# Kernel optimization log

Measured on AMD Instinct MI355X. Metric: run time of the kernel, lower is better.

## Reference

```python
import jax, jax.numpy as jnp
import numpy as np

V = 16384      # total nodes
G = 32         # nodes per graph (512 graphs)
D = 256        # node embedding dim == hidden_size
N = 8          # heads
H = 32         # head size
I = 1024       # intermediate size
LN_EPS = 1e-12


def _layer_norm(x, g, b):
    mu = jnp.mean(x, axis=-1, keepdims=True)
    var = jnp.mean(jnp.square(x - mu), axis=-1, keepdims=True)
    return (x - mu) * jax.lax.rsqrt(var + LN_EPS) * g + b


def setup_inputs() -> dict:
    key = jax.random.key(0)
    ks = jax.random.split(key, 5)
    node_embeddings = jax.random.normal(ks[0], (V, D), jnp.float32)
    # fully-connected pairs within each graph of size G (sorted by source node)
    idx = np.arange(V, dtype=np.int32).reshape(-1, G)          # [num_graphs, G]
    src = np.repeat(idx, G, axis=1).reshape(-1)                # [P]
    dst = np.tile(idx, (1, G)).reshape(-1)                     # [P]
    in_graph_node_pairs = jnp.asarray(np.stack([src, dst], axis=-1))  # [P, 2]
    s = 0.02
    return {
        "node_embeddings": node_embeddings,
        "in_graph_node_pairs": in_graph_node_pairs,
        "W_qkv": jax.random.normal(ks[1], (D, 3 * N * H), jnp.float32) * s,
        "W_o": jax.random.normal(ks[2], (N * H, D), jnp.float32) * s,
        "ln1_g": jnp.ones((D,), jnp.float32),
        "ln1_b": jnp.zeros((D,), jnp.float32),
        "W_i": jax.random.normal(ks[3], (D, I), jnp.float32) * s,
        "W_out2": jax.random.normal(ks[4], (I, D), jnp.float32) * s,
        "ln2_g": jnp.ones((D,), jnp.float32),
        "ln2_b": jnp.zeros((D,), jnp.float32),
    }


def reference(node_embeddings, in_graph_node_pairs, W_qkv, W_o, ln1_g, ln1_b,
              W_i, W_out2, ln2_g, ln2_b):
    nV = node_embeddings.shape[0]
    src = in_graph_node_pairs[:, 0]
    dst = in_graph_node_pairs[:, 1]
    # QKV projection -> [V, N, 3H] -> split
    qkv = (node_embeddings @ W_qkv).reshape(nV, N, 3 * H)
    q, k, v = jnp.split(qkv, 3, axis=-1)                       # each [V, N, H]
    # per-pair scores [P, N]
    scores = jnp.einsum('phi,phi->ph', q[src], k[dst]) / jnp.sqrt(jnp.float32(H))
    # segment softmax over source node, all heads at once
    m = jax.ops.segment_max(scores, src, num_segments=nV)       # [V, N]
    e = jnp.exp(scores - m[src])
    denom = jax.ops.segment_sum(e, src, num_segments=nV)        # [V, N]
    w = e / denom[src]                                          # [P, N]
    # weighted value scatter-sum -> [V, N, H]
    wv = w[:, :, None] * v[dst]
    att = jax.ops.segment_sum(wv, src, num_segments=nV).reshape(nV, N * H)
    # output projection + residual + LN
    pre = _layer_norm(att @ W_o + node_embeddings, ln1_g, ln1_b)
    inter = jax.nn.gelu(pre @ W_i, approximate=False)
    out = _layer_norm(inter @ W_out2 + pre, ln2_g, ln2_b)
    return out
```

## Files before the change

### kernel.cpp

```cpp
#include <hip/hip_runtime.h>
#include <math.h>

#define V 16384
#define D 256
#define NH 256
#define THREE_NH 768
#define IDIM 1024
#define LN_EPS 1e-12f
#define SCL 0.17677669529663687f

typedef short s16x8 __attribute__((ext_vector_type(8)));
typedef float f32x4 __attribute__((ext_vector_type(4)));

__device__ inline unsigned short f2bf(float f) {
    unsigned u = __float_as_uint(f);
    u += 0x7fffu + ((u >> 16) & 1u);
    return (unsigned short)(u >> 16);
}
__device__ inline float bf2f(unsigned short s) {
    return __uint_as_float(((unsigned)s) << 16);
}

__device__ inline float fast_erf(float x) {
    float ax = fabsf(x);
    float t  = 1.f / fmaf(0.3275911f, ax, 1.f);
    float p  = fmaf(fmaf(fmaf(fmaf(1.061405429f, t, -1.453152027f), t,
                              1.421413741f), t, -0.284496736f), t, 0.254829592f);
    float e  = 1.f - p * t * __expf(-ax * ax);
    return copysignf(e, x);
}

__device__ inline void gl2lds16(const unsigned short* g, unsigned short* l) {
    __builtin_amdgcn_global_load_lds(
        (__attribute__((address_space(1))) void*)(g),
        (__attribute__((address_space(3))) void*)(l), 16, 0, 0);
}

template <int ROWS_T>
__device__ inline void stage(const unsigned short* __restrict__ src, size_t row0,
                             int ldk, int k0, unsigned short* lds, int wv, int lane) {
    constexpr int PER_WAVE = ROWS_T / 32;
    #pragma unroll
    for (int i = 0; i < PER_WAVE; ++i) {
        const int seg = wv * PER_WAVE + i;
        const int r = seg * 8 + (lane >> 3);
        const int c = (lane & 7) ^ (r & 7);
        gl2lds16(src + (row0 + (size_t)r) * ldk + k0 + c * 8, lds + seg * 512);
    }
}

__device__ inline void stage_wp(const unsigned short* __restrict__ src, size_t row0,
                                int ldk, int k0, unsigned short* seg, int lane) {
    #pragma unroll
    for (int i = 0; i < 8; ++i) {
        const int r = i * 8 + (lane >> 3);
        const int c = (lane & 7) ^ (r & 7);
        gl2lds16(src + (row0 + (size_t)r) * ldk + k0 + c * 8, seg + i * 512);
    }
}

__device__ inline s16x8 fragld(const unsigned short* lds, int row, int chunk) {
    return *(const s16x8*)&lds[row * 64 + ((chunk ^ (row & 7)) << 3)];
}

#define WAVE_LGKM0() do { asm volatile("s_waitcnt lgkmcnt(0)" ::: "memory"); \
                          __builtin_amdgcn_sched_barrier(0); } while (0)
#define WAVE_VM0()   do { asm volatile("s_waitcnt vmcnt(0)" ::: "memory");   \
                          __builtin_amdgcn_sched_barrier(0); } while (0)

__global__ __launch_bounds__(256) void prep(const float* __restrict__ X,
                                            unsigned short* __restrict__ Xb,
                                            const float* __restrict__ Wqkv,
                                            const float* __restrict__ Wo,
                                            const float* __restrict__ Wi,
                                            const float* __restrict__ Wo2,
                                            unsigned short* __restrict__ WqkvT,
                                            unsigned short* __restrict__ WoT,
                                            unsigned short* __restrict__ WiT,
                                            unsigned short* __restrict__ Wo2T) {
    const int b = blockIdx.x, t = threadIdx.x;
    if (b >= 768) {
        int i = (b - 768) * 256 + t;
        float4 v = ((const float4*)X)[i];
        ushort4 o;
        o.x = f2bf(v.x); o.y = f2bf(v.y); o.z = f2bf(v.z); o.w = f2bf(v.w);
        ((ushort4*)Xb)[i] = o;
        return;
    }
    __shared__ float tile[32][33];
    const float* W; unsigned short* Wt; int K, N, bx, by;
    if (b < 192)      { W = Wqkv; Wt = WqkvT; K = 256;  N = 768;  bx = b & 7;          by = b >> 3; }
    else if (b < 256) { W = Wo;   Wt = WoT;   K = 256;  N = 256;  bx = (b - 192) & 7;  by = (b - 192) >> 3; }
    else if (b < 512) { W = Wi;   Wt = WiT;   K = 256;  N = 1024; bx = (b - 256) & 7;  by = (b - 256) >> 3; }
    else              { W = Wo2;  Wt = Wo2T;  K = 1024; N = 256;  bx = (b - 512) & 31; by = (b - 512) >> 5; }
    const int k0 = bx * 32, n0 = by * 32;
    #pragma unroll
    for (int p = 0; p < 4; ++p) {
        int idx = t + p * 256, r = idx >> 5, c = idx & 31;
        tile[r][c] = W[(size_t)(k0 + r) * N + n0 + c];
    }
    __syncthreads();
    #pragma unroll
    for (int p = 0; p < 4; ++p) {
        int idx = t + p * 256, r = idx >> 5, c = idx & 31;
        Wt[(size_t)(n0 + r) * K + k0 + c] = f2bf(tile[c][r]);
    }
}

template <int K, int N, int EPI>
__global__ __launch_bounds__(256) void gemm128(const unsigned short* __restrict__ A,
                                               const unsigned short* __restrict__ Bt,
                                               unsigned short* __restrict__ C) {
    __shared__ unsigned short As[128 * 64];
    __shared__ unsigned short Bs[128 * 64];
    constexpr int NCOL = N / 128;
    const int b = blockIdx.x;
    const int idx = b >> 3;
    const int r0 = ((b & 7) * 16 + idx / NCOL) * 128;
    const int c0 = (idx % NCOL) * 128;
    const int t = threadIdx.x;
    const int wv = t >> 6, lane = t & 63, q = lane >> 4, l16 = lane & 15;
    const int wr = (wv >> 1) * 64, wc = (wv & 1) * 64;
    f32x4 acc[4][4] = {};

    for (int k0 = 0; k0 < K; k0 += 64) {
        __syncthreads();
        stage<128>(A,  (size_t)r0, K, k0, As, wv, lane);
        stage<128>(Bt, (size_t)c0, K, k0, Bs, wv, lane);
        __builtin_amdgcn_s_waitcnt(0);
        __syncthreads();
        #pragma unroll
        for (int kk2 = 0; kk2 < 2; ++kk2) {
            s16x8 af[4], bfr[4];
            #pragma unroll
            for (int mf = 0; mf < 4; ++mf)
                af[mf] = fragld(As, wr + mf * 16 + l16, kk2 * 4 + q);
            #pragma unroll
            for (int nf = 0; nf < 4; ++nf)
                bfr[nf] = fragld(Bs, wc + nf * 16 + l16, kk2 * 4 + q);
            #pragma unroll
            for (int mf = 0; mf < 4; ++mf)
                #pragma unroll
                for (int nf = 0; nf < 4; ++nf)
                    acc[mf][nf] = __builtin_amdgcn_mfma_f32_16x16x32_bf16(af[mf], bfr[nf], acc[mf][nf], 0, 0, 0);
        }
    }

    #pragma unroll
    for (int mf = 0; mf < 4; ++mf)
        #pragma unroll
        for (int nf = 0; nf < 4; ++nf) {
            const int cg = c0 + wc + nf * 16 + l16;
            #pragma unroll
            for (int r = 0; r < 4; ++r) {
                const int rg = r0 + wr + mf * 16 + q * 4 + r;
                float v = acc[mf][nf][r];
                if (EPI == 1) v = 0.5f * v * (1.f + fast_erf(v * 0.70710678118654752f));
                C[(size_t)rg * N + cg] = f2bf(v);
            }
        }
}

__device__ inline void ffn_mfma8(const unsigned short* At, const unsigned short* Bb,
                                 int l16, int q, f32x4 (&acc)[2][4]) {
    #pragma unroll
    for (int kk2 = 0; kk2 < 2; ++kk2) {
        s16x8 af[2], bv[4];
        #pragma unroll
        for (int mf = 0; mf < 2; ++mf)
            af[mf] = fragld(At, mf * 16 + l16, kk2 * 4 + q);
        #pragma unroll
        for (int nf = 0; nf < 4; ++nf)
            bv[nf] = fragld(Bb, nf * 16 + l16, kk2 * 4 + q);
        #pragma unroll
        for (int mf = 0; mf < 2; ++mf)
            #pragma unroll
            for (int nf = 0; nf < 4; ++nf)
                acc[mf][nf] = __builtin_amdgcn_mfma_f32_16x16x32_bf16(af[mf], bv[nf], acc[mf][nf], 0, 0, 0);
    }
}

__global__ __launch_bounds__(256) void ffn_ln(const unsigned short* __restrict__ preb,
                                              const unsigned short* __restrict__ WiT,
                                              const unsigned short* __restrict__ Wo2T,
                                              const float* __restrict__ gamma,
                                              const float* __restrict__ beta,
                                              float* __restrict__ out) {
    __shared__ unsigned short Apre[8192];
    __shared__ unsigned short Bs[16384];
    __shared__ unsigned short Pbuf[8192];
    __shared__ float2 partial[4][32];
    __shared__ float2 stats[32];
    const int t = threadIdx.x, r0 = blockIdx.x * 32;
    const int wv = t >> 6, lane = t & 63, q = lane >> 4, l16 = lane & 15;
    const int wc = wv * 64;
    unsigned short* Bseg = Bs + wv * 4096;
    f32x4 acc2[2][4] = {};

    #pragma unroll
    for (int kc = 0; kc < 4; ++kc)
        stage<32>(preb, (size_t)r0, 256, kc * 64, Apre + kc * 2048, wv, lane);
    stage_wp(WiT, (size_t)wc, 256, 0, Bseg, lane);
    __builtin_amdgcn_s_waitcnt(0);
    __syncthreads();

    for (int nc = 0; nc < 4; ++nc) {
        const int ncn = (nc + 1) & 3;
        f32x4 acc1[2][4] = {};

        #pragma unroll
        for (int k0 = 0; k0 < 256; k0 += 64) {
            WAVE_VM0();
            ffn_mfma8(Apre + (k0 >> 6) * 2048, Bseg, l16, q, acc1);
            WAVE_LGKM0();
            if (k0 < 192)
                stage_wp(WiT, (size_t)(nc * 256 + wc), 256, k0 + 64, Bseg, lane);
            else
                stage_wp(Wo2T, (size_t)wc, IDIM, nc * 256, Bseg, lane);
        }

        #pragma unroll
        for (int mf = 0; mf < 2; ++mf)
            #pragma unroll
            for (int nf = 0; nf < 4; ++nf)
                #pragma unroll
                for (int r = 0; r < 4; ++r) {
                    float v = acc1[mf][nf][r];
                    v = 0.5f * v * (1.f + fast_erf(v * 0.70710678118654752f));
                    const int i = mf * 16 + q * 4 + r;
                    const int colc = wc + nf * 16 + l16;
                    const int c8 = (colc >> 3) & 7;
                    Pbuf[wv * 2048 + i * 64 + ((c8 ^ (i & 7)) << 3) + (colc & 7)] = f2bf(v);
                }
        __syncthreads();

        #pragma unroll
        for (int ks = 0; ks < 256; ks += 64) {
            WAVE_VM0();
            ffn_mfma8(Pbuf + (ks >> 6) * 2048, Bseg, l16, q, acc2);
            WAVE_LGKM0();
            if (ks < 192)
                stage_wp(Wo2T, (size_t)wc, IDIM, nc * 256 + ks + 64, Bseg, lane);
            else
                stage_wp(WiT, (size_t)(ncn * 256 + wc), 256, 0, Bseg, lane);
        }
        __syncthreads();
    }

    #pragma unroll
    for (int mf = 0; mf < 2; ++mf)
        #pragma unroll
        for (int nf = 0; nf < 4; ++nf) {
            const int cg = wc + nf * 16 + l16;
            const int kb = cg >> 6, c8 = (cg >> 3) & 7, e = cg & 7;
            #pragma unroll
            for (int r = 0; r < 4; ++r) {
                const int i = mf * 16 + q * 4 + r;
                acc2[mf][nf][r] += bf2f(Apre[kb * 2048 + i * 64 + ((c8 ^ (i & 7)) << 3) + e]);
            }
        }

    #pragma unroll
    for (int mf = 0; mf < 2; ++mf) {
        float s[4] = {0.f, 0.f, 0.f, 0.f}, ss[4] = {0.f, 0.f, 0.f, 0.f};
        #pragma unroll
        for (int nf = 0; nf < 4; ++nf)
            #pragma unroll
            for (int r = 0; r < 4; ++r) {
                float v = acc2[mf][nf][r];
                s[r] += v; ss[r] += v * v;
            }
        #pragma unroll
        for (int off = 1; off < 16; off <<= 1)
            #pragma unroll
            for (int r = 0; r < 4; ++r) {
                s[r]  += __shfl_xor(s[r],  off);
                ss[r] += __shfl_xor(ss[r], off);
            }
        if (l16 == 0)
            #pragma unroll
            for (int r = 0; r < 4; ++r)
                partial[wv][mf * 16 + q * 4 + r] = make_float2(s[r], ss[r]);
    }
    __syncthreads();
    if (t < 32) {
        float s = 0.f, ss = 0.f;
        #pragma unroll
        for (int w = 0; w < 4; ++w) { s += partial[w][t].x; ss += partial[w][t].y; }
        float mu  = s * (1.f / 256.f);
        float var = ss * (1.f / 256.f) - mu * mu;
        stats[t] = make_float2(mu, rsqrtf(var + LN_EPS));
    }
    __syncthreads();

    #pragma unroll
    for (int mf = 0; mf < 2; ++mf)
        #pragma unroll
        for (int nf = 0; nf < 4; ++nf) {
            const int cg = wc + nf * 16 + l16;
            const float g = gamma[cg], b = beta[cg];
            #pragma unroll
            for (int r = 0; r < 4; ++r) {
                const int rl = mf * 16 + q * 4 + r;
                const float2 st = stats[rl];
                out[(size_t)(r0 + rl) * NH + cg] = (acc2[mf][nf][r] - st.x) * st.y * g + b;
            }
        }
}

__global__ __launch_bounds__(256) void attln(const unsigned short* __restrict__ qkv,
                                             const unsigned short* __restrict__ WoT,
                                             const float* __restrict__ X,
                                             const float* __restrict__ gamma,
                                             const float* __restrict__ beta,
                                             unsigned short* __restrict__ preb) {
    __shared__ unsigned short smem[25216];
    unsigned short* Ks = smem;
    unsigned short* Vt = smem + 8192;
    unsigned short* Ps = smem + 16384;
    unsigned short* at = smem;
    unsigned short* Bs = smem + 8192;
    float2* partial = (float2*)(smem + 24576);
    float2* stats   = (float2*)(smem + 24576 + 512);

    const int g = blockIdx.x, t = threadIdx.x;
    const int wv = t >> 6, lane = t & 63, q = lane >> 4, l16 = lane & 15;
    const unsigned short* src = qkv + (size_t)g * 32 * THREE_NH;

    s16x8 qf[2][2];
    #pragma unroll
    for (int hh = 0; hh < 2; ++hh)
        #pragma unroll
        for (int mf = 0; mf < 2; ++mf)
            qf[hh][mf] = *(const s16x8*)&src[(size_t)(mf * 16 + l16) * THREE_NH +
                                             (wv * 2 + hh) * 96 + q * 8];

    s16x8 vld[4];
    int vh[4], vj[4], vdc[4];
    #pragma unroll
    for (int i = 0; i < 4; ++i) {
        int cid = i * 256 + t;
        vh[i] = cid >> 7; int rem = cid & 127; vj[i] = rem >> 2; vdc[i] = rem & 3;
        vld[i] = *(const s16x8*)&src[(size_t)vj[i] * THREE_NH + vh[i] * 96 + 64 + vdc[i] * 8];
    }

    #pragma unroll
    for (int i = 0; i < 4; ++i) {
        int ck = (wv * 4 + i) * 64 + lane;
        int h = ck >> 7, j = (ck >> 2) & 31, c = ck & 3;
        gl2lds16(src + (size_t)j * THREE_NH + h * 96 + 32 + c * 8, Ks + (wv * 4 + i) * 512);
    }

    #pragma unroll
    for (int i = 0; i < 4; ++i)
        #pragma unroll
        for (int e = 0; e < 8; ++e) {
            int d = vdc[i] * 8 + e;
            Vt[vh[i] * 1024 + d * 32 + ((((vj[i] >> 3) ^ ((d >> 2) & 3))) << 3) + (vj[i] & 7)] =
                (unsigned short)vld[i][e];
        }

    __builtin_amdgcn_s_waitcnt(0);
    __syncthreads();

    f32x4 sacc[2][2][2] = {};
    #pragma unroll
    for (int hh = 0; hh < 2; ++hh) {
        const int h = wv * 2 + hh;
        #pragma unroll
        for (int nf = 0; nf < 2; ++nf) {
            s16x8 kf = *(const s16x8*)&Ks[h * 1024 + (nf * 16 + l16) * 32 + q * 8];
            #pragma unroll
            for (int mf = 0; mf < 2; ++mf)
                sacc[hh][mf][nf] = __builtin_amdgcn_mfma_f32_16x16x32_bf16(
                    qf[hh][mf], kf, sacc[hh][mf][nf], 0, 0, 0);
        }
    }

    float inv[2][2][4];
    #pragma unroll
    for (int hh = 0; hh < 2; ++hh) {
        const int h = wv * 2 + hh;
        #pragma unroll
        for (int mf = 0; mf < 2; ++mf)
            #pragma unroll
            for (int r = 0; r < 4; ++r) {
                float a0 = sacc[hh][mf][0][r], a1 = sacc[hh][mf][1][r];
                float m = fmaxf(a0, a1);
                m = fmaxf(m, __shfl_xor(m, 1));
                m = fmaxf(m, __shfl_xor(m, 2));
                m = fmaxf(m, __shfl_xor(m, 4));
                m = fmaxf(m, __shfl_xor(m, 8));
                float e0 = __expf((a0 - m) * SCL);
                float e1 = __expf((a1 - m) * SCL);
                float sm = e0 + e1;
                sm += __shfl_xor(sm, 1);
                sm += __shfl_xor(sm, 2);
                sm += __shfl_xor(sm, 4);
                sm += __shfl_xor(sm, 8);
                inv[hh][mf][r] = 1.f / sm;
                const int row = mf * 16 + q * 4 + r;
                const int base = h * 1024 + row * 32 + (l16 & 7);
                Ps[base + ((((l16 >> 3) ^ q)) << 3)]       = f2bf(e0);
                Ps[base + ((((2 + (l16 >> 3)) ^ q)) << 3)] = f2bf(e1);
            }
    }

    f32x4 oacc[2][2][2] = {};
    #pragma unroll
    for (int hh = 0; hh < 2; ++hh) {
        const int h = wv * 2 + hh;
        const int sw = (l16 >> 2) & 3;
        s16x8 pa[2], vb[2];
        #pragma unroll
        for (int mf = 0; mf < 2; ++mf)
            pa[mf] = *(const s16x8*)&Ps[h * 1024 + (mf * 16 + l16) * 32 + ((q ^ sw) << 3)];
        #pragma unroll
        for (int nf = 0; nf < 2; ++nf)
            vb[nf] = *(const s16x8*)&Vt[h * 1024 + (nf * 16 + l16) * 32 + ((q ^ sw) << 3)];
        #pragma unroll
        for (int mf = 0; mf < 2; ++mf)
            #pragma unroll
            for (int nf = 0; nf < 2; ++nf)
                oacc[hh][mf][nf] = __builtin_amdgcn_mfma_f32_16x16x32_bf16(
                    pa[mf], vb[nf], oacc[hh][mf][nf], 0, 0, 0);
    }
    __syncthreads();

    const int wc = wv * 64;
    unsigned short* Bseg = Bs + wv * 4096;
    stage_wp(WoT, (size_t)wc, 256, 0, Bseg, lane);

    #pragma unroll
    for (int hh = 0; hh < 2; ++hh)
        #pragma unroll
        for (int mf = 0; mf < 2; ++mf)
            #pragma unroll
            for (int nf = 0; nf < 2; ++nf)
                #pragma unroll
                for (int r = 0; r < 4; ++r) {
                    float val = oacc[hh][mf][nf][r] * inv[hh][mf][r];
                    const int i = mf * 16 + q * 4 + r;
                    const int col = (wv * 2 + hh) * 32 + nf * 16 + l16;
                    const int kb = col >> 6, c = (col >> 3) & 7;
                    at[kb * 2048 + i * 64 + ((c ^ (i & 7)) << 3) + (col & 7)] = f2bf(val);
                }
    __syncthreads();

    const int r0 = g * 32;
    f32x4 acc[2][4] = {};

    #pragma unroll
    for (int kc = 0; kc < 4; ++kc) {
        WAVE_VM0();
        const unsigned short* atk = at + kc * 2048;
        #pragma unroll
        for (int kk2 = 0; kk2 < 2; ++kk2) {
            s16x8 af[2], bv[4];
            #pragma unroll
            for (int mf = 0; mf < 2; ++mf)
                af[mf] = fragld(atk, mf * 16 + l16, kk2 * 4 + q);
            #pragma unroll
            for (int nf = 0; nf < 4; ++nf)
                bv[nf] = fragld(Bseg, nf * 16 + l16, kk2 * 4 + q);
            #pragma unroll
            for (int mf = 0; mf < 2; ++mf)
                #pragma unroll
                for (int nf = 0; nf < 4; ++nf)
                    acc[mf][nf] = __builtin_amdgcn_mfma_f32_16x16x32_bf16(af[mf], bv[nf], acc[mf][nf], 0, 0, 0);
        }
        if (kc < 3) {
            WAVE_LGKM0();
            stage_wp(WoT, (size_t)wc, 256, (kc + 1) * 64, Bseg, lane);
        }
    }

    #pragma unroll
    for (int mf = 0; mf < 2; ++mf)
        #pragma unroll
        for (int nf = 0; nf < 4; ++nf) {
            const int cg = wc + nf * 16 + l16;
            #pragma unroll
            for (int r = 0; r < 4; ++r)
                acc[mf][nf][r] += X[(size_t)(r0 + mf * 16 + q * 4 + r) * NH + cg];
        }

    #pragma unroll
    for (int mf = 0; mf < 2; ++mf) {
        float sp[4] = {0.f, 0.f, 0.f, 0.f}, ssp[4] = {0.f, 0.f, 0.f, 0.f};
        #pragma unroll
        for (int nf = 0; nf < 4; ++nf)
            #pragma unroll
            for (int r = 0; r < 4; ++r) {
                float v = acc[mf][nf][r];
                sp[r] += v; ssp[r] += v * v;
            }
        #pragma unroll
        for (int off = 1; off < 16; off <<= 1)
            #pragma unroll
            for (int r = 0; r < 4; ++r) {
                sp[r]  += __shfl_xor(sp[r],  off);
                ssp[r] += __shfl_xor(ssp[r], off);
            }
        if (l16 == 0)
            #pragma unroll
            for (int r = 0; r < 4; ++r)
                partial[wv * 32 + mf * 16 + q * 4 + r] = make_float2(sp[r], ssp[r]);
    }
    __syncthreads();
    if (t < 32) {
        float sv = 0.f, ssv = 0.f;
        #pragma unroll
        for (int w = 0; w < 4; ++w) { sv += partial[w * 32 + t].x; ssv += partial[w * 32 + t].y; }
        float mu  = sv * (1.f / 256.f);
        float var = ssv * (1.f / 256.f) - mu * mu;
        stats[t] = make_float2(mu, rsqrtf(var + LN_EPS));
    }
    __syncthreads();

    #pragma unroll
    for (int mf = 0; mf < 2; ++mf)
        #pragma unroll
        for (int nf = 0; nf < 4; ++nf) {
            const int cg = wc + nf * 16 + l16;
            const float gm = gamma[cg], bt = beta[cg];
            #pragma unroll
            for (int r = 0; r < 4; ++r) {
                const int rl = mf * 16 + q * 4 + r;
                const float2 st = stats[rl];
                float v = (acc[mf][nf][r] - st.x) * st.y * gm + bt;
                preb[(size_t)(r0 + rl) * NH + cg] = f2bf(v);
            }
        }
}

extern "C" void kernel_launch(void* const* d_in, const int* in_sizes, int n_in,
                              void* d_out, int out_size, void* d_ws, size_t ws_size,
                              hipStream_t stream) {
    const float* X      = (const float*)d_in[0];
    const float* W_qkv  = (const float*)d_in[2];
    const float* W_o    = (const float*)d_in[3];
    const float* ln1_g  = (const float*)d_in[4];
    const float* ln1_b  = (const float*)d_in[5];
    const float* W_i    = (const float*)d_in[6];
    const float* W_out2 = (const float*)d_in[7];
    const float* ln2_g  = (const float*)d_in[8];
    const float* ln2_b  = (const float*)d_in[9];
    float* out = (float*)d_out;

    char* ws = (char*)d_ws;
    unsigned short* Xbf   = (unsigned short*)(ws);
    unsigned short* qkvb  = (unsigned short*)(ws + 8388608);
    unsigned short* preb  = (unsigned short*)(ws + 58720256);
    unsigned short* WqkvT = (unsigned short*)(ws + 67108864);
    unsigned short* WoT   = (unsigned short*)(ws + 67502080);
    unsigned short* WiT   = (unsigned short*)(ws + 67633152);
    unsigned short* Wo2T  = (unsigned short*)(ws + 68157440);

    dim3 blk(256);
    hipLaunchKernelGGL(prep, dim3(768 + V * D / 4 / 256), blk, 0, stream,
                       X, Xbf, W_qkv, W_o, W_i, W_out2, WqkvT, WoT, WiT, Wo2T);

    hipLaunchKernelGGL((gemm128<D, THREE_NH, 0>), dim3(V / 128 * (THREE_NH / 128)), blk, 0, stream,
                       Xbf, WqkvT, qkvb);
    hipLaunchKernelGGL(attln, dim3(V / 32), blk, 0, stream,
                       qkvb, WoT, X, ln1_g, ln1_b, preb);
    hipLaunchKernelGGL(ffn_ln, dim3(V / 32), blk, 0, stream,
                       preb, WiT, Wo2T, ln2_g, ln2_b, out);
}
```

Before: 153.7 us.

## Split fused FFN+LN kernel across eight waves with 32-column slices

The fused FFN/LayerNorm kernel now launches 512 threads per block instead of 256, so each of eight waves owns a 32-column slice instead of a 64-column slice. Per-wave weight staging, MFMA tiles, the GELU buffer indexing and the LN partial reduction are all adjusted to match. The goal is more waves in flight to hide global-to-LDS latency and raise MFMA utilisation. In exchange each wave reuses its A fragments across fewer columns, and per-block LDS use stays the same while the thread count doubles.

```diff
diff --git a/kernel.cpp b/kernel.cpp
--- a/kernel.cpp
+++ b/kernel.cpp
@@ -53,6 +53,16 @@
                                 int ldk, int k0, unsigned short* seg, int lane) {
     #pragma unroll
     for (int i = 0; i < 8; ++i) {
+        const int r = i * 8 + (lane >> 3);
+        const int c = (lane & 7) ^ (r & 7);
+        gl2lds16(src + (row0 + (size_t)r) * ldk + k0 + c * 8, seg + i * 512);
+    }
+}
+
+__device__ inline void stage_wp32(const unsigned short* __restrict__ src, size_t row0,
+                                  int ldk, int k0, unsigned short* seg, int lane) {
+    #pragma unroll
+    for (int i = 0; i < 4; ++i) {
         const int r = i * 8 + (lane >> 3);
         const int c = (lane & 7) ^ (r & 7);
         gl2lds16(src + (row0 + (size_t)r) * ldk + k0 + c * 8, seg + i * 512);
@@ -161,26 +171,26 @@
         }
 }
 
-__device__ inline void ffn_mfma8(const unsigned short* At, const unsigned short* Bb,
-                                 int l16, int q, f32x4 (&acc)[2][4]) {
+__device__ inline void ffn_mfma4(const unsigned short* At, const unsigned short* Bb,
+                                 int l16, int q, f32x4 (&acc)[2][2]) {
     #pragma unroll
     for (int kk2 = 0; kk2 < 2; ++kk2) {
-        s16x8 af[2], bv[4];
+        s16x8 af[2], bv[2];
         #pragma unroll
         for (int mf = 0; mf < 2; ++mf)
             af[mf] = fragld(At, mf * 16 + l16, kk2 * 4 + q);
         #pragma unroll
-        for (int nf = 0; nf < 4; ++nf)
+        for (int nf = 0; nf < 2; ++nf)
             bv[nf] = fragld(Bb, nf * 16 + l16, kk2 * 4 + q);
         #pragma unroll
         for (int mf = 0; mf < 2; ++mf)
             #pragma unroll
-            for (int nf = 0; nf < 4; ++nf)
+            for (int nf = 0; nf < 2; ++nf)
                 acc[mf][nf] = __builtin_amdgcn_mfma_f32_16x16x32_bf16(af[mf], bv[nf], acc[mf][nf], 0, 0, 0);
     }
 }
 
-__global__ __launch_bounds__(256) void ffn_ln(const unsigned short* __restrict__ preb,
+__global__ __launch_bounds__(512) void ffn_ln(const unsigned short* __restrict__ preb,
                                               const unsigned short* __restrict__ WiT,
                                               const unsigned short* __restrict__ Wo2T,
                                               const float* __restrict__ gamma,
@@ -189,60 +199,65 @@
     __shared__ unsigned short Apre[8192];
     __shared__ unsigned short Bs[16384];
     __shared__ unsigned short Pbuf[8192];
-    __shared__ float2 partial[4][32];
+    __shared__ float2 partial[8][32];
     __shared__ float2 stats[32];
     const int t = threadIdx.x, r0 = blockIdx.x * 32;
     const int wv = t >> 6, lane = t & 63, q = lane >> 4, l16 = lane & 15;
-    const int wc = wv * 64;
-    unsigned short* Bseg = Bs + wv * 4096;
-    f32x4 acc2[2][4] = {};
-
-    #pragma unroll
-    for (int kc = 0; kc < 4; ++kc)
-        stage<32>(preb, (size_t)r0, 256, kc * 64, Apre + kc * 2048, wv, lane);
-    stage_wp(WiT, (size_t)wc, 256, 0, Bseg, lane);
+    const int wc = wv * 32;
+    unsigned short* Bseg = Bs + wv * 2048;
+    f32x4 acc2[2][2] = {};
+
+    #pragma unroll
+    for (int i = 0; i < 2; ++i) {
+        const int seg = wv * 2 + i;
+        const int kb = seg >> 2, sub = seg & 3;
+        const int r = sub * 8 + (lane >> 3);
+        const int c = (lane & 7) ^ (r & 7);
+        gl2lds16(preb + (size_t)(r0 + r) * 256 + kb * 64 + c * 8, Apre + seg * 512);
+    }
+    stage_wp32(WiT, (size_t)wc, 256, 0, Bseg, lane);
     __builtin_amdgcn_s_waitcnt(0);
     __syncthreads();
 
     for (int nc = 0; nc < 4; ++nc) {
         const int ncn = (nc + 1) & 3;
-        f32x4 acc1[2][4] = {};
+        f32x4 acc1[2][2] = {};
 
         #pragma unroll
         for (int k0 = 0; k0 < 256; k0 += 64) {
             WAVE_VM0();
-            ffn_mfma8(Apre + (k0 >> 6) * 2048, Bseg, l16, q, acc1);
+            ffn_mfma4(Apre + (k0 >> 6) * 2048, Bseg, l16, q, acc1);
             WAVE_LGKM0();
             if (k0 < 192)
-                stage_wp(WiT, (size_t)(nc * 256 + wc), 256, k0 + 64, Bseg, lane);
+                stage_wp32(WiT, (size_t)(nc * 256 + wc), 256, k0 + 64, Bseg, lane);
             else
-                stage_wp(Wo2T, (size_t)wc, IDIM, nc * 256, Bseg, lane);
-        }
-
-        #pragma unroll
-        for (int mf = 0; mf < 2; ++mf)
-            #pragma unroll
-            for (int nf = 0; nf < 4; ++nf)
+                stage_wp32(Wo2T, (size_t)wc, IDIM, nc * 256, Bseg, lane);
+        }
+
+        #pragma unroll
+        for (int mf = 0; mf < 2; ++mf)
+            #pragma unroll
+            for (int nf = 0; nf < 2; ++nf)
                 #pragma unroll
                 for (int r = 0; r < 4; ++r) {
                     float v = acc1[mf][nf][r];
                     v = 0.5f * v * (1.f + fast_erf(v * 0.70710678118654752f));
                     const int i = mf * 16 + q * 4 + r;
                     const int colc = wc + nf * 16 + l16;
-                    const int c8 = (colc >> 3) & 7;
-                    Pbuf[wv * 2048 + i * 64 + ((c8 ^ (i & 7)) << 3) + (colc & 7)] = f2bf(v);
+                    Pbuf[(colc >> 6) * 2048 + i * 64 +
+                         ((((colc >> 3) & 7) ^ (i & 7)) << 3) + (colc & 7)] = f2bf(v);
                 }
         __syncthreads();
 
         #pragma unroll
         for (int ks = 0; ks < 256; ks += 64) {
             WAVE_VM0();
-            ffn_mfma8(Pbuf + (ks >> 6) * 2048, Bseg, l16, q, acc2);
+            ffn_mfma4(Pbuf + (ks >> 6) * 2048, Bseg, l16, q, acc2);
             WAVE_LGKM0();
             if (ks < 192)
-                stage_wp(Wo2T, (size_t)wc, IDIM, nc * 256 + ks + 64, Bseg, lane);
+                stage_wp32(Wo2T, (size_t)wc, IDIM, nc * 256 + ks + 64, Bseg, lane);
             else
-                stage_wp(WiT, (size_t)(ncn * 256 + wc), 256, 0, Bseg, lane);
+                stage_wp32(WiT, (size_t)(ncn * 256 + wc), 256, 0, Bseg, lane);
         }
         __syncthreads();
     }
@@ -250,7 +265,7 @@
     #pragma unroll
     for (int mf = 0; mf < 2; ++mf)
         #pragma unroll
-        for (int nf = 0; nf < 4; ++nf) {
+        for (int nf = 0; nf < 2; ++nf) {
             const int cg = wc + nf * 16 + l16;
             const int kb = cg >> 6, c8 = (cg >> 3) & 7, e = cg & 7;
             #pragma unroll
@@ -264,7 +279,7 @@
     for (int mf = 0; mf < 2; ++mf) {
         float s[4] = {0.f, 0.f, 0.f, 0.f}, ss[4] = {0.f, 0.f, 0.f, 0.f};
         #pragma unroll
-        for (int nf = 0; nf < 4; ++nf)
+        for (int nf = 0; nf < 2; ++nf)
             #pragma unroll
             for (int r = 0; r < 4; ++r) {
                 float v = acc2[mf][nf][r];
@@ -286,7 +301,7 @@
     if (t < 32) {
         float s = 0.f, ss = 0.f;
         #pragma unroll
-        for (int w = 0; w < 4; ++w) { s += partial[w][t].x; ss += partial[w][t].y; }
+        for (int w = 0; w < 8; ++w) { s += partial[w][t].x; ss += partial[w][t].y; }
         float mu  = s * (1.f / 256.f);
         float var = ss * (1.f / 256.f) - mu * mu;
         stats[t] = make_float2(mu, rsqrtf(var + LN_EPS));
@@ -296,7 +311,7 @@
     #pragma unroll
     for (int mf = 0; mf < 2; ++mf)
         #pragma unroll
-        for (int nf = 0; nf < 4; ++nf) {
+        for (int nf = 0; nf < 2; ++nf) {
             const int cg = wc + nf * 16 + l16;
             const float g = gamma[cg], b = beta[cg];
             #pragma unroll
@@ -565,6 +580,6 @@
                        Xbf, WqkvT, qkvb);
     hipLaunchKernelGGL(attln, dim3(V / 32), blk, 0, stream,
                        qkvb, WoT, X, ln1_g, ln1_b, preb);
-    hipLaunchKernelGGL(ffn_ln, dim3(V / 32), blk, 0, stream,
+    hipLaunchKernelGGL(ffn_ln, dim3(V / 32), dim3(512), 0, stream,
                        preb, WiT, Wo2T, ln2_g, ln2_b, out);
 }
```

Measured after the change: 167.2 us. +8.8%, slower.

## Fuse attention+LN1 kernel with FFN+LN2 kernel into one per-graph kernel

Applied to the files above, without the earlier changes.

Merges the attention/output-projection/LN1 kernel and the FFN/LN2 kernel into a single kernel. The normalized pre-FFN activation stays in shared memory as bf16 instead of being written to and reread from global memory, and one launch is removed. Shared memory per block grows from about 50KB to about 67KB, which may lower occupancy, and the fused kernel may use more registers.

```diff
diff --git a/kernel.cpp b/kernel.cpp
--- a/kernel.cpp
+++ b/kernel.cpp
@@ -180,152 +180,35 @@
     }
 }
 
-__global__ __launch_bounds__(256) void ffn_ln(const unsigned short* __restrict__ preb,
+__global__ __launch_bounds__(256) void attffn(const unsigned short* __restrict__ qkv,
+                                              const unsigned short* __restrict__ WoT,
+                                              const float* __restrict__ X,
+                                              const float* __restrict__ ln1g,
+                                              const float* __restrict__ ln1b,
                                               const unsigned short* __restrict__ WiT,
                                               const unsigned short* __restrict__ Wo2T,
-                                              const float* __restrict__ gamma,
-                                              const float* __restrict__ beta,
+                                              const float* __restrict__ ln2g,
+                                              const float* __restrict__ ln2b,
                                               float* __restrict__ out) {
-    __shared__ unsigned short Apre[8192];
-    __shared__ unsigned short Bs[16384];
-    __shared__ unsigned short Pbuf[8192];
-    __shared__ float2 partial[4][32];
-    __shared__ float2 stats[32];
-    const int t = threadIdx.x, r0 = blockIdx.x * 32;
-    const int wv = t >> 6, lane = t & 63, q = lane >> 4, l16 = lane & 15;
-    const int wc = wv * 64;
-    unsigned short* Bseg = Bs + wv * 4096;
-    f32x4 acc2[2][4] = {};
-
-    #pragma unroll
-    for (int kc = 0; kc < 4; ++kc)
-        stage<32>(preb, (size_t)r0, 256, kc * 64, Apre + kc * 2048, wv, lane);
-    stage_wp(WiT, (size_t)wc, 256, 0, Bseg, lane);
-    __builtin_amdgcn_s_waitcnt(0);
-    __syncthreads();
-
-    for (int nc = 0; nc < 4; ++nc) {
-        const int ncn = (nc + 1) & 3;
-        f32x4 acc1[2][4] = {};
-
-        #pragma unroll
-        for (int k0 = 0; k0 < 256; k0 += 64) {
-            WAVE_VM0();
-            ffn_mfma8(Apre + (k0 >> 6) * 2048, Bseg, l16, q, acc1);
-            WAVE_LGKM0();
-            if (k0 < 192)
-                stage_wp(WiT, (size_t)(nc * 256 + wc), 256, k0 + 64, Bseg, lane);
-            else
-                stage_wp(Wo2T, (size_t)wc, IDIM, nc * 256, Bseg, lane);
-        }
-
-        #pragma unroll
-        for (int mf = 0; mf < 2; ++mf)
-            #pragma unroll
-            for (int nf = 0; nf < 4; ++nf)
-                #pragma unroll
-                for (int r = 0; r < 4; ++r) {
-                    float v = acc1[mf][nf][r];
-                    v = 0.5f * v * (1.f + fast_erf(v * 0.70710678118654752f));
-                    const int i = mf * 16 + q * 4 + r;
-                    const int colc = wc + nf * 16 + l16;
-                    const int c8 = (colc >> 3) & 7;
-                    Pbuf[wv * 2048 + i * 64 + ((c8 ^ (i & 7)) << 3) + (colc & 7)] = f2bf(v);
-                }
-        __syncthreads();
-
-        #pragma unroll
-        for (int ks = 0; ks < 256; ks += 64) {
-            WAVE_VM0();
-            ffn_mfma8(Pbuf + (ks >> 6) * 2048, Bseg, l16, q, acc2);
-            WAVE_LGKM0();
-            if (ks < 192)
-                stage_wp(Wo2T, (size_t)wc, IDIM, nc * 256 + ks + 64, Bseg, lane);
-            else
-                stage_wp(WiT, (size_t)(ncn * 256 + wc), 256, 0, Bseg, lane);
-        }
-        __syncthreads();
-    }
-
-    #pragma unroll
-    for (int mf = 0; mf < 2; ++mf)
-        #pragma unroll
-        for (int nf = 0; nf < 4; ++nf) {
-            const int cg = wc + nf * 16 + l16;
-            const int kb = cg >> 6, c8 = (cg >> 3) & 7, e = cg & 7;
-            #pragma unroll
-            for (int r = 0; r < 4; ++r) {
-                const int i = mf * 16 + q * 4 + r;
-                acc2[mf][nf][r] += bf2f(Apre[kb * 2048 + i * 64 + ((c8 ^ (i & 7)) << 3) + e]);
-            }
-        }
-
-    #pragma unroll
-    for (int mf = 0; mf < 2; ++mf) {
-        float s[4] = {0.f, 0.f, 0.f, 0.f}, ss[4] = {0.f, 0.f, 0.f, 0.f};
-        #pragma unroll
-        for (int nf = 0; nf < 4; ++nf)
-            #pragma unroll
-            for (int r = 0; r < 4; ++r) {
-                float v = acc2[mf][nf][r];
-                s[r] += v; ss[r] += v * v;
-            }
-        #pragma unroll
-        for (int off = 1; off < 16; off <<= 1)
-            #pragma unroll
-            for (int r = 0; r < 4; ++r) {
-                s[r]  += __shfl_xor(s[r],  off);
-                ss[r] += __shfl_xor(ss[r], off);
-            }
-        if (l16 == 0)
-            #pragma unroll
-            for (int r = 0; r < 4; ++r)
-                partial[wv][mf * 16 + q * 4 + r] = make_float2(s[r], ss[r]);
-    }
-    __syncthreads();
-    if (t < 32) {
-        float s = 0.f, ss = 0.f;
-        #pragma unroll
-        for (int w = 0; w < 4; ++w) { s += partial[w][t].x; ss += partial[w][t].y; }
-        float mu  = s * (1.f / 256.f);
-        float var = ss * (1.f / 256.f) - mu * mu;
-        stats[t] = make_float2(mu, rsqrtf(var + LN_EPS));
-    }
-    __syncthreads();
-
-    #pragma unroll
-    for (int mf = 0; mf < 2; ++mf)
-        #pragma unroll
-        for (int nf = 0; nf < 4; ++nf) {
-            const int cg = wc + nf * 16 + l16;
-            const float g = gamma[cg], b = beta[cg];
-            #pragma unroll
-            for (int r = 0; r < 4; ++r) {
-                const int rl = mf * 16 + q * 4 + r;
-                const float2 st = stats[rl];
-                out[(size_t)(r0 + rl) * NH + cg] = (acc2[mf][nf][r] - st.x) * st.y * g + b;
-            }
-        }
-}
-
-__global__ __launch_bounds__(256) void attln(const unsigned short* __restrict__ qkv,
-                                             const unsigned short* __restrict__ WoT,
-                                             const float* __restrict__ X,
-                                             const float* __restrict__ gamma,
-                                             const float* __restrict__ beta,
-                                             unsigned short* __restrict__ preb) {
-    __shared__ unsigned short smem[25216];
+    __shared__ unsigned short smem[33408];
     unsigned short* Ks = smem;
     unsigned short* Vt = smem + 8192;
     unsigned short* Ps = smem + 16384;
     unsigned short* at = smem;
-    unsigned short* Bs = smem + 8192;
-    float2* partial = (float2*)(smem + 24576);
-    float2* stats   = (float2*)(smem + 24576 + 512);
+    unsigned short* Bsp = smem + 8192;
+    unsigned short* Apre = smem;
+    unsigned short* Pbuf = smem + 24576;
+    float2* partial1 = (float2*)(smem + 24576);
+    float2* stats1   = (float2*)(smem + 24576 + 512);
+    float2* partial2 = (float2*)(smem + 32768);
+    float2* stats2   = (float2*)(smem + 32768 + 512);
 
     const int g = blockIdx.x, t = threadIdx.x;
     const int wv = t >> 6, lane = t & 63, q = lane >> 4, l16 = lane & 15;
     const unsigned short* src = qkv + (size_t)g * 32 * THREE_NH;
+    const int wc = wv * 64;
+    const int r0 = g * 32;
+    unsigned short* Bseg = Bsp + wv * 4096;
 
     s16x8 qf[2][2];
     #pragma unroll
@@ -427,8 +310,6 @@
     }
     __syncthreads();
 
-    const int wc = wv * 64;
-    unsigned short* Bseg = Bs + wv * 4096;
     stage_wp(WoT, (size_t)wc, 256, 0, Bseg, lane);
 
     #pragma unroll
@@ -447,32 +328,139 @@
                 }
     __syncthreads();
 
-    const int r0 = g * 32;
-    f32x4 acc[2][4] = {};
-
-    #pragma unroll
-    for (int kc = 0; kc < 4; ++kc) {
-        WAVE_VM0();
-        const unsigned short* atk = at + kc * 2048;
-        #pragma unroll
-        for (int kk2 = 0; kk2 < 2; ++kk2) {
-            s16x8 af[2], bv[4];
-            #pragma unroll
-            for (int mf = 0; mf < 2; ++mf)
-                af[mf] = fragld(atk, mf * 16 + l16, kk2 * 4 + q);
+    {
+        f32x4 acc[2][4] = {};
+        #pragma unroll
+        for (int kc = 0; kc < 4; ++kc) {
+            WAVE_VM0();
+            const unsigned short* atk = at + kc * 2048;
+            #pragma unroll
+            for (int kk2 = 0; kk2 < 2; ++kk2) {
+                s16x8 af[2], bv[4];
+                #pragma unroll
+                for (int mf = 0; mf < 2; ++mf)
+                    af[mf] = fragld(atk, mf * 16 + l16, kk2 * 4 + q);
+                #pragma unroll
+                for (int nf = 0; nf < 4; ++nf)
+                    bv[nf] = fragld(Bseg, nf * 16 + l16, kk2 * 4 + q);
+                #pragma unroll
+                for (int mf = 0; mf < 2; ++mf)
+                    #pragma unroll
+                    for (int nf = 0; nf < 4; ++nf)
+                        acc[mf][nf] = __builtin_amdgcn_mfma_f32_16x16x32_bf16(af[mf], bv[nf], acc[mf][nf], 0, 0, 0);
+            }
+            if (kc < 3) {
+                WAVE_LGKM0();
+                stage_wp(WoT, (size_t)wc, 256, (kc + 1) * 64, Bseg, lane);
+            }
+        }
+
+        #pragma unroll
+        for (int mf = 0; mf < 2; ++mf)
+            #pragma unroll
+            for (int nf = 0; nf < 4; ++nf) {
+                const int cg = wc + nf * 16 + l16;
+                #pragma unroll
+                for (int r = 0; r < 4; ++r)
+                    acc[mf][nf][r] += X[(size_t)(r0 + mf * 16 + q * 4 + r) * NH + cg];
+            }
+
+        #pragma unroll
+        for (int mf = 0; mf < 2; ++mf) {
+            float sp[4] = {0.f, 0.f, 0.f, 0.f}, ssp[4] = {0.f, 0.f, 0.f, 0.f};
             #pragma unroll
             for (int nf = 0; nf < 4; ++nf)
-                bv[nf] = fragld(Bseg, nf * 16 + l16, kk2 * 4 + q);
-            #pragma unroll
-            for (int mf = 0; mf < 2; ++mf)
-                #pragma unroll
-                for (int nf = 0; nf < 4; ++nf)
-                    acc[mf][nf] = __builtin_amdgcn_mfma_f32_16x16x32_bf16(af[mf], bv[nf], acc[mf][nf], 0, 0, 0);
-        }
-        if (kc < 3) {
+                #pragma unroll
+                for (int r = 0; r < 4; ++r) {
+                    float v = acc[mf][nf][r];
+                    sp[r] += v; ssp[r] += v * v;
+                }
+            #pragma unroll
+            for (int off = 1; off < 16; off <<= 1)
+                #pragma unroll
+                for (int r = 0; r < 4; ++r) {
+                    sp[r]  += __shfl_xor(sp[r],  off);
+                    ssp[r] += __shfl_xor(ssp[r], off);
+                }
+            if (l16 == 0)
+                #pragma unroll
+                for (int r = 0; r < 4; ++r)
+                    partial1[wv * 32 + mf * 16 + q * 4 + r] = make_float2(sp[r], ssp[r]);
+        }
+        __syncthreads();
+        if (t < 32) {
+            float sv = 0.f, ssv = 0.f;
+            #pragma unroll
+            for (int w = 0; w < 4; ++w) { sv += partial1[w * 32 + t].x; ssv += partial1[w * 32 + t].y; }
+            float mu  = sv * (1.f / 256.f);
+            float var = ssv * (1.f / 256.f) - mu * mu;
+            stats1[t] = make_float2(mu, rsqrtf(var + LN_EPS));
+        }
+        __syncthreads();
+
+        #pragma unroll
+        for (int mf = 0; mf < 2; ++mf)
+            #pragma unroll
+            for (int nf = 0; nf < 4; ++nf) {
+                const int cg = wc + nf * 16 + l16;
+                const float gm = ln1g[cg], bt = ln1b[cg];
+                const int kb = cg >> 6, c8 = (cg >> 3) & 7, e = cg & 7;
+                #pragma unroll
+                for (int r = 0; r < 4; ++r) {
+                    const int i = mf * 16 + q * 4 + r;
+                    const float2 st = stats1[i];
+                    float v = (acc[mf][nf][r] - st.x) * st.y * gm + bt;
+                    Apre[kb * 2048 + i * 64 + ((c8 ^ (i & 7)) << 3) + e] = f2bf(v);
+                }
+            }
+    }
+    stage_wp(WiT, (size_t)wc, 256, 0, Bseg, lane);
+    WAVE_LGKM0();
+    __builtin_amdgcn_s_barrier();
+    __builtin_amdgcn_sched_barrier(0);
+
+    f32x4 acc2[2][4] = {};
+    for (int nc = 0; nc < 4; ++nc) {
+        const int ncn = (nc + 1) & 3;
+        f32x4 acc1[2][4] = {};
+
+        #pragma unroll
+        for (int k0 = 0; k0 < 256; k0 += 64) {
+            WAVE_VM0();
+            ffn_mfma8(Apre + (k0 >> 6) * 2048, Bseg, l16, q, acc1);
             WAVE_LGKM0();
-            stage_wp(WoT, (size_t)wc, 256, (kc + 1) * 64, Bseg, lane);
-        }
+            if (k0 < 192)
+                stage_wp(WiT, (size_t)(nc * 256 + wc), 256, k0 + 64, Bseg, lane);
+            else
+                stage_wp(Wo2T, (size_t)wc, IDIM, nc * 256, Bseg, lane);
+        }
+
+        #pragma unroll
+        for (int mf = 0; mf < 2; ++mf)
+            #pragma unroll
+            for (int nf = 0; nf < 4; ++nf)
+                #pragma unroll
+                for (int r = 0; r < 4; ++r) {
+                    float v = acc1[mf][nf][r];
+                    v = 0.5f * v * (1.f + fast_erf(v * 0.70710678118654752f));
+                    const int i = mf * 16 + q * 4 + r;
+                    const int colc = wc + nf * 16 + l16;
+                    const int c8 = (colc >> 3) & 7;
+                    Pbuf[wv * 2048 + i * 64 + ((c8 ^ (i & 7)) << 3) + (colc & 7)] = f2bf(v);
+                }
+        __syncthreads();
+
+        #pragma unroll
+        for (int ks = 0; ks < 256; ks += 64) {
+            WAVE_VM0();
+            ffn_mfma8(Pbuf + (ks >> 6) * 2048, Bseg, l16, q, acc2);
+            WAVE_LGKM0();
+            if (ks < 192)
+                stage_wp(Wo2T, (size_t)wc, IDIM, nc * 256 + ks + 64, Bseg, lane);
+            else
+                stage_wp(WiT, (size_t)(ncn * 256 + wc), 256, 0, Bseg, lane);
+        }
+        __syncthreads();
     }
 
     #pragma unroll
@@ -480,41 +468,44 @@
         #pragma unroll
         for (int nf = 0; nf < 4; ++nf) {
             const int cg = wc + nf * 16 + l16;
+            const int kb = cg >> 6, c8 = (cg >> 3) & 7, e = cg & 7;
+            #pragma unroll
+            for (int r = 0; r < 4; ++r) {
+                const int i = mf * 16 + q * 4 + r;
+                acc2[mf][nf][r] += bf2f(Apre[kb * 2048 + i * 64 + ((c8 ^ (i & 7)) << 3) + e]);
+            }
+        }
+
+    #pragma unroll
+    for (int mf = 0; mf < 2; ++mf) {
+        float s[4] = {0.f, 0.f, 0.f, 0.f}, ss[4] = {0.f, 0.f, 0.f, 0.f};
+        #pragma unroll
+        for (int nf = 0; nf < 4; ++nf)
+            #pragma unroll
+            for (int r = 0; r < 4; ++r) {
+                float v = acc2[mf][nf][r];
+                s[r] += v; ss[r] += v * v;
+            }
+        #pragma unroll
+        for (int off = 1; off < 16; off <<= 1)
+            #pragma unroll
+            for (int r = 0; r < 4; ++r) {
+                s[r]  += __shfl_xor(s[r],  off);
+                ss[r] += __shfl_xor(ss[r], off);
+            }
+        if (l16 == 0)
             #pragma unroll
             for (int r = 0; r < 4; ++r)
-                acc[mf][nf][r] += X[(size_t)(r0 + mf * 16 + q * 4 + r) * NH + cg];
-        }
-
-    #pragma unroll
-    for (int mf = 0; mf < 2; ++mf) {
-        float sp[4] = {0.f, 0.f, 0.f, 0.f}, ssp[4] = {0.f, 0.f, 0.f, 0.f};
-        #pragma unroll
-        for (int nf = 0; nf < 4; ++nf)
-            #pragma unroll
-            for (int r = 0; r < 4; ++r) {
-                float v = acc[mf][nf][r];
-                sp[r] += v; ssp[r] += v * v;
-            }
-        #pragma unroll
-        for (int off = 1; off < 16; off <<= 1)
-            #pragma unroll
-            for (int r = 0; r < 4; ++r) {
-                sp[r]  += __shfl_xor(sp[r],  off);
-                ssp[r] += __shfl_xor(ssp[r], off);
-            }
-        if (l16 == 0)
-            #pragma unroll
-            for (int r = 0; r < 4; ++r)
-                partial[wv * 32 + mf * 16 + q * 4 + r] = make_float2(sp[r], ssp[r]);
+                partial2[wv * 32 + mf * 16 + q * 4 + r] = make_float2(s[r], ss[r]);
     }
     __syncthreads();
     if (t < 32) {
-        float sv = 0.f, ssv = 0.f;
-        #pragma unroll
-        for (int w = 0; w < 4; ++w) { sv += partial[w * 32 + t].x; ssv += partial[w * 32 + t].y; }
-        float mu  = sv * (1.f / 256.f);
-        float var = ssv * (1.f / 256.f) - mu * mu;
-        stats[t] = make_float2(mu, rsqrtf(var + LN_EPS));
+        float s = 0.f, ss = 0.f;
+        #pragma unroll
+        for (int w = 0; w < 4; ++w) { s += partial2[w * 32 + t].x; ss += partial2[w * 32 + t].y; }
+        float mu  = s * (1.f / 256.f);
+        float var = ss * (1.f / 256.f) - mu * mu;
+        stats2[t] = make_float2(mu, rsqrtf(var + LN_EPS));
     }
     __syncthreads();
 
@@ -523,13 +514,12 @@
         #pragma unroll
         for (int nf = 0; nf < 4; ++nf) {
             const int cg = wc + nf * 16 + l16;
-            const float gm = gamma[cg], bt = beta[cg];
+            const float gm = ln2g[cg], bt = ln2b[cg];
             #pragma unroll
             for (int r = 0; r < 4; ++r) {
                 const int rl = mf * 16 + q * 4 + r;
-                const float2 st = stats[rl];
-                float v = (acc[mf][nf][r] - st.x) * st.y * gm + bt;
-                preb[(size_t)(r0 + rl) * NH + cg] = f2bf(v);
+                const float2 st = stats2[rl];
+                out[(size_t)(r0 + rl) * NH + cg] = (acc2[mf][nf][r] - st.x) * st.y * gm + bt;
             }
         }
 }
@@ -551,7 +541,6 @@
     char* ws = (char*)d_ws;
     unsigned short* Xbf   = (unsigned short*)(ws);
     unsigned short* qkvb  = (unsigned short*)(ws + 8388608);
-    unsigned short* preb  = (unsigned short*)(ws + 58720256);
     unsigned short* WqkvT = (unsigned short*)(ws + 67108864);
     unsigned short* WoT   = (unsigned short*)(ws + 67502080);
     unsigned short* WiT   = (unsigned short*)(ws + 67633152);
@@ -563,8 +552,6 @@
 
     hipLaunchKernelGGL((gemm128<D, THREE_NH, 0>), dim3(V / 128 * (THREE_NH / 128)), blk, 0, stream,
                        Xbf, WqkvT, qkvb);
-    hipLaunchKernelGGL(attln, dim3(V / 32), blk, 0, stream,
-                       qkvb, WoT, X, ln1_g, ln1_b, preb);
-    hipLaunchKernelGGL(ffn_ln, dim3(V / 32), blk, 0, stream,
-                       preb, WiT, Wo2T, ln2_g, ln2_b, out);
-}
+    hipLaunchKernelGGL(attffn, dim3(V / 32), blk, 0, stream,
+                       qkvb, WoT, X, ln1_g, ln1_b, WiT, Wo2T, ln2_g, ln2_b, out);
+}
```

Result: slower. 190.2 us (+23.8%).
